# Kernel tuning notes

Measured on AMD Instinct MI355X. Metric: run time of the kernel, lower is better.

The kernel has to match this reference:

```python
import jax, jax.numpy as jnp
import numpy as np

HEADS = 16
DIM_HEAD = 64
SCALE = DIM_HEAD ** -0.5
MASK_NEG = 1000000.0


def setup_inputs() -> dict:
    key = jax.random.key(0)
    ks = jax.random.split(key, 6)
    B, N, M, D = 2, 2048, 2048, 1024
    inner = HEADS * DIM_HEAD  # 1024
    x = jax.random.normal(ks[0], (B, N, D), dtype=jnp.float32)
    context = jax.random.normal(ks[1], (B, M, D), dtype=jnp.float32)
    mask = jax.random.randint(ks[2], (B, N), 0, 2, dtype=jnp.int32)
    Wq = jax.random.normal(ks[3], (D, inner), dtype=jnp.float32) * (D ** -0.5)
    Wkv = jax.random.normal(ks[4], (D, 2 * inner), dtype=jnp.float32) * (D ** -0.5)
    Wout = jax.random.normal(ks[5], (inner, D), dtype=jnp.float32) * (inner ** -0.5)
    bout = jnp.zeros((D,), dtype=jnp.float32)
    return {"x": x, "context": context, "mask": mask,
            "Wq": Wq, "Wkv": Wkv, "Wout": Wout, "bout": bout}


def _split_heads(t):
    # [b, n, (h d)] -> [b, h, n, d]
    b, n, _ = t.shape
    return t.reshape(b, n, HEADS, DIM_HEAD).transpose(0, 2, 1, 3)


def reference(x, context, mask, Wq, Wkv, Wout, bout):
    kv = context @ Wkv                      # [b, m, 2*inner]
    k, v = jnp.split(kv, 2, axis=-1)
    q = x @ Wq                              # [b, n, inner]
    q, k, v = _split_heads(q), _split_heads(k), _split_heads(v)
    dots = jnp.einsum('bhnd,bhmd->bhnm', q, k) * SCALE
    # mask is [b, n]: additive penalty per query row (faithful to source)
    dots = dots - (1.0 - mask.astype(jnp.float32))[:, None, :, None] * MASK_NEG
    attn = jax.nn.softmax(dots, axis=-1)
    out = jnp.einsum('bhnm,bhmd->bhnd', attn, v)  # [b, h, n, d]
    b, h, n, d = out.shape
    out = out.transpose(0, 2, 1, 3).reshape(b, n, h * d)
    return out @ Wout + bout
```

## Files before the change

kernel.cpp:

```cpp
#include <hip/hip_runtime.h>
#include <hip/hip_bf16.h>
#include <math.h>

#define BATCH   2
#define NQ      2048
#define NKV     2048
#define DMODEL  1024
#define HEADS   16
#define INNER   1024
#define KVCOLS  2048

typedef short bf16x8 __attribute__((ext_vector_type(8)));
typedef float f32x4  __attribute__((ext_vector_type(4)));

__device__ __forceinline__ short f2bf(float x) {
    __hip_bfloat16 h = __float2bfloat16(x);
    return *reinterpret_cast<short*>(&h);
}
__device__ __forceinline__ float bf2f(short h) {
    unsigned int u = ((unsigned int)(unsigned short)h) << 16;
    float f;
    __builtin_memcpy(&f, &u, 4);
    return f;
}
__device__ __forceinline__ void gl_lds16(const void* g, void* l) {
    __builtin_amdgcn_global_load_lds(
        (const __attribute__((address_space(1))) unsigned int*)g,
        (__attribute__((address_space(3))) unsigned int*)l, 16, 0, 0);
}
__device__ __forceinline__ int sw(int row, int chunk) {
    return row * 64 + ((chunk ^ (row & 7)) << 3);
}

__global__ __launch_bounds__(256)
void split_cast(const float* __restrict__ in, short* __restrict__ hi,
                short* __restrict__ lo, int n)
{
    int i = (blockIdx.x * 256 + threadIdx.x) * 4;
    if (i >= n) return;
    float4 v = *(const float4*)(in + i);
    short4 h, l;
    h.x = f2bf(v.x); l.x = f2bf(v.x - bf2f(h.x));
    h.y = f2bf(v.y); l.y = f2bf(v.y - bf2f(h.y));
    h.z = f2bf(v.z); l.z = f2bf(v.z - bf2f(h.z));
    h.w = f2bf(v.w); l.w = f2bf(v.w - bf2f(h.w));
    *(short4*)(hi + i) = h;
    *(short4*)(lo + i) = l;
}

__device__ __forceinline__ void tile_transpose_split(
    const float* __restrict__ W, short* __restrict__ Wth, short* __restrict__ Wtl,
    int Kd, int Nd, int bx, int by, int split)
{
    __shared__ float t[32][33];
    const int lx = threadIdx.x & 31, ly = threadIdx.x >> 5;
    #pragma unroll
    for (int j = 0; j < 4; ++j)
        t[ly + j * 8][lx] = W[(size_t)(by * 32 + ly + j * 8) * Nd + bx * 32 + lx];
    __syncthreads();
    #pragma unroll
    for (int j = 0; j < 4; ++j) {
        const float v = t[lx][ly + j * 8];
        const short h = f2bf(v);
        const size_t idx = (size_t)(bx * 32 + ly + j * 8) * Kd + by * 32 + lx;
        Wth[idx] = h;
        if (split) Wtl[idx] = f2bf(v - bf2f(h));
    }
}

__global__ __launch_bounds__(256)
void prep_weights(const float* __restrict__ Wq, const float* __restrict__ Wkv,
                  const float* __restrict__ Wout,
                  short* __restrict__ WqTh, short* __restrict__ WqTl,
                  short* __restrict__ WkvTh, short* __restrict__ WkvTl,
                  short* __restrict__ WoutT)
{
    const int id = blockIdx.x;
    if (id < 1024) {
        tile_transpose_split(Wq, WqTh, WqTl, 1024, 1024, id & 31, id >> 5, 1);
    } else if (id < 3072) {
        const int r = id - 1024;
        tile_transpose_split(Wkv, WkvTh, WkvTl, 1024, 2048, r & 63, r >> 6, 1);
    } else {
        const int r = id - 3072;
        tile_transpose_split(Wout, WoutT, nullptr, 1024, 1024, r & 31, r >> 5, 0);
    }
}

template <int MODE>
__global__ __launch_bounds__(256)
void gemm3(const short* __restrict__ Ah, const short* __restrict__ Al,
           const short* __restrict__ Bth, const short* __restrict__ Btl,
           short* __restrict__ Chi, short* __restrict__ Clo,
           int Md, int Nd, int Kd)
{
    __shared__ short Ash[64 * 64];
    __shared__ short Asl[64 * 64];
    __shared__ short Bsh[64 * 64];
    __shared__ short Bsl[64 * 64];
    const int tid = threadIdx.x;
    const int m0 = blockIdx.y * 64, n0 = blockIdx.x * 64;
    const int w = tid >> 6, ln = tid & 63;
    const int wm = (w & 1) * 32, wn = (w >> 1) * 32;
    const int lr = ln & 15, lq = ln >> 4;

    f32x4 acc[2][2];
    #pragma unroll
    for (int mt = 0; mt < 2; ++mt)
        #pragma unroll
        for (int nt = 0; nt < 2; ++nt)
            #pragma unroll
            for (int r = 0; r < 4; ++r) acc[mt][nt][r] = 0.0f;

    for (int k0 = 0; k0 < Kd; k0 += 64) {
        __syncthreads();
        #pragma unroll
        for (int it = 0; it < 2; ++it) {
            const int f = it * 256 + tid;
            const int row = f >> 3, c8 = f & 7;
            gl_lds16(Ah  + (size_t)(m0 + row) * Kd + k0 + c8 * 8, Ash + f * 8);
            gl_lds16(Al  + (size_t)(m0 + row) * Kd + k0 + c8 * 8, Asl + f * 8);
            gl_lds16(Bth + (size_t)(n0 + row) * Kd + k0 + c8 * 8, Bsh + f * 8);
            gl_lds16(Btl + (size_t)(n0 + row) * Kd + k0 + c8 * 8, Bsl + f * 8);
        }
        __syncthreads();

        #pragma unroll
        for (int ks = 0; ks < 2; ++ks) {
            bf16x8 ah[2], al[2], bh[2], bl[2];
            #pragma unroll
            for (int t = 0; t < 2; ++t) {
                ah[t] = *(const bf16x8*)(Ash + (wm + t * 16 + lr) * 64 + ks * 32 + lq * 8);
                al[t] = *(const bf16x8*)(Asl + (wm + t * 16 + lr) * 64 + ks * 32 + lq * 8);
                bh[t] = *(const bf16x8*)(Bsh + (wn + t * 16 + lr) * 64 + ks * 32 + lq * 8);
                bl[t] = *(const bf16x8*)(Bsl + (wn + t * 16 + lr) * 64 + ks * 32 + lq * 8);
            }
            #pragma unroll
            for (int mt = 0; mt < 2; ++mt)
                #pragma unroll
                for (int nt = 0; nt < 2; ++nt) {
                    acc[mt][nt] = __builtin_amdgcn_mfma_f32_16x16x32_bf16(
                        ah[mt], bh[nt], acc[mt][nt], 0, 0, 0);
                    acc[mt][nt] = __builtin_amdgcn_mfma_f32_16x16x32_bf16(
                        ah[mt], bl[nt], acc[mt][nt], 0, 0, 0);
                    acc[mt][nt] = __builtin_amdgcn_mfma_f32_16x16x32_bf16(
                        al[mt], bh[nt], acc[mt][nt], 0, 0, 0);
                }
        }
    }

    #pragma unroll
    for (int mt = 0; mt < 2; ++mt)
        #pragma unroll
        for (int nt = 0; nt < 2; ++nt)
            #pragma unroll
            for (int r = 0; r < 4; ++r) {
                const int row = m0 + wm + mt * 16 + lq * 4 + r;
                const int col = n0 + wn + nt * 16 + lr;
                float v = acc[mt][nt][r];
                if (MODE == 1) v *= 0.125f;
                const short hh = f2bf(v);
                Chi[(size_t)row * Nd + col] = hh;
                Clo[(size_t)row * Nd + col] = f2bf(v - bf2f(hh));
            }
}

template <int FOUT>
__global__ __launch_bounds__(256)
void gemm1(const short* __restrict__ A, const short* __restrict__ Bt,
           void* __restrict__ Cv, int Md, int Nd, int Kd,
           const float* __restrict__ bias)
{
    __shared__ short As[64 * 64];
    __shared__ short Bs[64 * 64];
    const int tid = threadIdx.x;
    const int m0 = blockIdx.y * 64, n0 = blockIdx.x * 64;
    const int w = tid >> 6, ln = tid & 63;
    const int wm = (w & 1) * 32, wn = (w >> 1) * 32;
    const int lr = ln & 15, lq = ln >> 4;

    f32x4 acc[2][2];
    #pragma unroll
    for (int mt = 0; mt < 2; ++mt)
        #pragma unroll
        for (int nt = 0; nt < 2; ++nt)
            #pragma unroll
            for (int r = 0; r < 4; ++r) acc[mt][nt][r] = 0.0f;

    for (int k0 = 0; k0 < Kd; k0 += 64) {
        __syncthreads();
        #pragma unroll
        for (int it = 0; it < 2; ++it) {
            const int f = it * 256 + tid;
            const int row = f >> 3, c8 = f & 7;
            gl_lds16(A  + (size_t)(m0 + row) * Kd + k0 + c8 * 8, As + f * 8);
            gl_lds16(Bt + (size_t)(n0 + row) * Kd + k0 + c8 * 8, Bs + f * 8);
        }
        __syncthreads();
        #pragma unroll
        for (int ks = 0; ks < 2; ++ks) {
            bf16x8 af[2], bfr[2];
            #pragma unroll
            for (int t = 0; t < 2; ++t) {
                af[t]  = *(const bf16x8*)(As + (wm + t * 16 + lr) * 64 + ks * 32 + lq * 8);
                bfr[t] = *(const bf16x8*)(Bs + (wn + t * 16 + lr) * 64 + ks * 32 + lq * 8);
            }
            #pragma unroll
            for (int mt = 0; mt < 2; ++mt)
                #pragma unroll
                for (int nt = 0; nt < 2; ++nt)
                    acc[mt][nt] = __builtin_amdgcn_mfma_f32_16x16x32_bf16(
                        af[mt], bfr[nt], acc[mt][nt], 0, 0, 0);
        }
    }
    #pragma unroll
    for (int mt = 0; mt < 2; ++mt)
        #pragma unroll
        for (int nt = 0; nt < 2; ++nt)
            #pragma unroll
            for (int r = 0; r < 4; ++r) {
                const int row = m0 + wm + mt * 16 + lq * 4 + r;
                const int col = n0 + wn + nt * 16 + lr;
                if (FOUT == 1)
                    ((float*)Cv)[(size_t)row * Nd + col] = acc[mt][nt][r] + bias[col];
                else
                    ((short*)Cv)[(size_t)row * Nd + col] = f2bf(acc[mt][nt][r]);
            }
}

__global__ __launch_bounds__(512, 4)
void flash_v5(const short* __restrict__ qh, const short* __restrict__ ql,
              const short* __restrict__ kh, const short* __restrict__ kl,
              const short* __restrict__ vp, const int* __restrict__ mask,
              short* __restrict__ aob)
{
    const int qt = blockIdx.x, h = blockIdx.y, b = blockIdx.z;
    const int tid = threadIdx.x;
    const int w = tid >> 6, ln = tid & 63;
    const int lr = ln & 15, lq = ln >> 4;

    __shared__ short Kh[2 * 4096];
    __shared__ short Kl[2 * 4096];
    __shared__ short Vt[2 * 4096];
    __shared__ short Ps[128 * 64];

    const size_t qrow0 = (size_t)(b * NQ + qt * 128);

    bf16x8 aqh[2], aql[2];
    #pragma unroll
    for (int ks = 0; ks < 2; ++ks) {
        const size_t qoff = (qrow0 + w * 16 + lr) * INNER + h * 64 + ks * 32 + lq * 8;
        aqh[ks] = *(const bf16x8*)(qh + qoff);
        aql[ks] = *(const bf16x8*)(ql + qoff);
    }
    float keep[4];
    #pragma unroll
    for (int r = 0; r < 4; ++r)
        keep[r] = (float)mask[b * NQ + qt * 128 + w * 16 + lq * 4 + r];

    const int srow = tid >> 3, sc8 = tid & 7;
    const int kdst = sw(srow, sc8);
    const int kp = tid & 31, dg4 = (tid >> 5) * 4;
    int4 rkh, rkl; int2 rva, rvb;

    {
        const size_t koff = (size_t)(b * NKV + srow) * INNER + h * 64 + sc8 * 8;
        rkh = *(const int4*)(kh + koff);
        rkl = *(const int4*)(kl + koff);
        const short* v0 = vp + (size_t)(b * NKV + 2 * kp) * INNER + h * 64 + dg4;
        rva = *(const int2*)(v0);
        rvb = *(const int2*)(v0 + INNER);
        *(int4*)(Kh + kdst) = rkh;
        *(int4*)(Kl + kdst) = rkl;
        const short* as = (const short*)&rva;
        const short* bs = (const short*)&rvb;
        int* vt32 = (int*)Vt;
        #pragma unroll
        for (int j = 0; j < 4; ++j)
            vt32[(dg4 + j) * 32 + (((kp >> 2) ^ ((dg4 + j) & 7)) << 2) + (kp & 3)] =
                (int)((unsigned short)as[j] | ((unsigned int)(unsigned short)bs[j] << 16));
    }

    float psum[4];
    #pragma unroll
    for (int r = 0; r < 4; ++r) psum[r] = 0.0f;
    f32x4 oacc[4];
    #pragma unroll
    for (int dg = 0; dg < 4; ++dg)
        #pragma unroll
        for (int r = 0; r < 4; ++r) oacc[dg][r] = 0.0f;

    for (int kt = 0; kt < NKV / 64; ++kt) {
        const int cur = kt & 1;
        if (kt < NKV / 64 - 1) {
            const size_t krow0 = (size_t)(b * NKV + (kt + 1) * 64);
            const size_t koff = (krow0 + srow) * INNER + h * 64 + sc8 * 8;
            rkh = *(const int4*)(kh + koff);
            rkl = *(const int4*)(kl + koff);
            const short* v0 = vp + (krow0 + 2 * kp) * INNER + h * 64 + dg4;
            rva = *(const int2*)(v0);
            rvb = *(const int2*)(v0 + INNER);
        }
        __syncthreads();

        const short* KhC = Kh + cur * 4096;
        const short* KlC = Kl + cur * 4096;
        const short* VtC = Vt + cur * 4096;

        f32x4 sacc[4];
        #pragma unroll
        for (int g = 0; g < 4; ++g)
            #pragma unroll
            for (int r = 0; r < 4; ++r) sacc[g][r] = 0.0f;
        #pragma unroll
        for (int ks = 0; ks < 2; ++ks) {
            #pragma unroll
            for (int g = 0; g < 4; ++g) {
                const bf16x8 bkh = *(const bf16x8*)(KhC + sw(g * 16 + lr, ks * 4 + lq));
                const bf16x8 bkl = *(const bf16x8*)(KlC + sw(g * 16 + lr, ks * 4 + lq));
                sacc[g] = __builtin_amdgcn_mfma_f32_16x16x32_bf16(aqh[ks], bkh, sacc[g], 0, 0, 0);
                sacc[g] = __builtin_amdgcn_mfma_f32_16x16x32_bf16(aqh[ks], bkl, sacc[g], 0, 0, 0);
                sacc[g] = __builtin_amdgcn_mfma_f32_16x16x32_bf16(aql[ks], bkh, sacc[g], 0, 0, 0);
            }
        }

        #pragma unroll
        for (int r = 0; r < 4; ++r) {
            const int prow = w * 16 + lq * 4 + r;
            #pragma unroll
            for (int g = 0; g < 4; ++g) {
                float s = sacc[g][r];
                if (keep[r] == 0.0f) s = rintf(s * 16.0f) * 0.0625f;
                const float p = __expf(s);
                psum[r] += p;
                Ps[sw(prow, g * 2 + (lr >> 3)) + (lr & 7)] = f2bf(p);
            }
        }

        #pragma unroll
        for (int ks = 0; ks < 2; ++ks) {
            const bf16x8 ap = *(const bf16x8*)(Ps + sw(w * 16 + lr, ks * 4 + lq));
            #pragma unroll
            for (int dg = 0; dg < 4; ++dg) {
                const bf16x8 bv = *(const bf16x8*)(VtC + sw(dg * 16 + lr, ks * 4 + lq));
                oacc[dg] = __builtin_amdgcn_mfma_f32_16x16x32_bf16(ap, bv, oacc[dg], 0, 0, 0);
            }
        }

        if (kt < NKV / 64 - 1) {
            short* KhN = Kh + (cur ^ 1) * 4096;
            short* KlN = Kl + (cur ^ 1) * 4096;
            *(int4*)(KhN + kdst) = rkh;
            *(int4*)(KlN + kdst) = rkl;
            const short* as = (const short*)&rva;
            const short* bs = (const short*)&rvb;
            int* vt32 = (int*)(Vt + (cur ^ 1) * 4096);
            #pragma unroll
            for (int j = 0; j < 4; ++j)
                vt32[(dg4 + j) * 32 + (((kp >> 2) ^ ((dg4 + j) & 7)) << 2) + (kp & 3)] =
                    (int)((unsigned short)as[j] | ((unsigned int)(unsigned short)bs[j] << 16));
        }
    }

    #pragma unroll
    for (int off = 1; off < 16; off <<= 1)
        #pragma unroll
        for (int r = 0; r < 4; ++r)
            psum[r] += __shfl_xor(psum[r], off, 64);

    #pragma unroll
    for (int dg = 0; dg < 4; ++dg)
        #pragma unroll
        for (int r = 0; r < 4; ++r) {
            const int row = w * 16 + lq * 4 + r;
            aob[(qrow0 + row) * INNER + h * 64 + dg * 16 + lr] =
                f2bf(oacc[dg][r] / psum[r]);
        }
}

extern "C" void kernel_launch(void* const* d_in, const int* in_sizes, int n_in,
                              void* d_out, int out_size, void* d_ws, size_t ws_size,
                              hipStream_t stream)
{
    const float* x    = (const float*)d_in[0];
    const float* ctx  = (const float*)d_in[1];
    const int*   mask = (const int*)d_in[2];
    const float* Wq   = (const float*)d_in[3];
    const float* Wkv  = (const float*)d_in[4];
    const float* Wout = (const float*)d_in[5];
    const float* bout = (const float*)d_in[6];
    float* out = (float*)d_out;

    short* base  = (short*)d_ws;
    short* xh    = base;
    short* xl    = base + (size_t)4 * 1024 * 1024;
    short* ch    = xh;
    short* cl    = xl;
    short* vp    = xl;
    short* aob   = xh;
    short* WqTh  = base + (size_t) 8 * 1024 * 1024;
    short* WqTl  = base + (size_t) 9 * 1024 * 1024;
    short* qhp   = base + (size_t)10 * 1024 * 1024;
    short* qlp   = base + (size_t)14 * 1024 * 1024;
    short* WkvTh = base + (size_t)18 * 1024 * 1024;
    short* WkvTl = base + (size_t)20 * 1024 * 1024;
    short* khp   = base + (size_t)22 * 1024 * 1024;
    short* klp   = base + (size_t)26 * 1024 * 1024;
    short* WoutT = base + (size_t)30 * 1024 * 1024;

    const dim3 blk(256);
    split_cast<<<4096, blk, 0, stream>>>(x, xh, xl, 4096 * 1024);
    prep_weights<<<4096, blk, 0, stream>>>(Wq, Wkv, Wout,
                                           WqTh, WqTl, WkvTh, WkvTl, WoutT);
    gemm3<1><<<dim3(1024 / 64, 4096 / 64), blk, 0, stream>>>(
        xh, xl, WqTh, WqTl, qhp, qlp, 4096, 1024, 1024);
    split_cast<<<4096, blk, 0, stream>>>(ctx, ch, cl, 4096 * 1024);
    gemm3<0><<<dim3(1024 / 64, 4096 / 64), blk, 0, stream>>>(
        ch, cl, WkvTh, WkvTl, khp, klp, 4096, 1024, 1024);
    gemm1<0><<<dim3(1024 / 64, 4096 / 64), blk, 0, stream>>>(
        ch, WkvTh + (size_t)1024 * 1024, vp, 4096, 1024, 1024, nullptr);
    flash_v5<<<dim3(NQ / 128, HEADS, BATCH), dim3(512), 0, stream>>>(
        qhp, qlp, khp, klp, vp, mask, aob);
    gemm1<1><<<dim3(1024 / 64, 4096 / 64), blk, 0, stream>>>(
        aob, WoutT, out, 4096, 1024, 1024, bout);
}
```

Baseline: 308.7 us.

## Fuse prep kernels and batch Q/K/V projections into one larger-tile GEMM

Merges the two split_cast launches and the weight transpose into one prep kernel. Replaces three separate 64x64-tile projection GEMMs with a single launch that uses blockIdx.z to select Q, K or V. The new kernel uses 128x128 tiles with a 32-wide K step and an XOR-swizzled LDS layout, and V skips the low-part terms. Context and V get their own workspace buffers so the projections can run concurrently. This is meant to cut launch count, raise per-block data reuse and fill the GPU better, at the cost of more registers per thread (16 accumulators) and possibly lower occupancy.

```diff
diff --git a/kernel.cpp b/kernel.cpp
--- a/kernel.cpp
+++ b/kernel.cpp
@@ -32,12 +32,11 @@
     return row * 64 + ((chunk ^ (row & 7)) << 3);
 }
 
-__global__ __launch_bounds__(256)
-void split_cast(const float* __restrict__ in, short* __restrict__ hi,
-                short* __restrict__ lo, int n)
-{
-    int i = (blockIdx.x * 256 + threadIdx.x) * 4;
-    if (i >= n) return;
+__device__ __forceinline__ void split_chunk(const float* __restrict__ in,
+                                            short* __restrict__ hi,
+                                            short* __restrict__ lo, int id)
+{
+    const int i = (id * 256 + (int)threadIdx.x) * 4;
     float4 v = *(const float4*)(in + i);
     short4 h, l;
     h.x = f2bf(v.x); l.x = f2bf(v.x - bf2f(h.x));
@@ -69,78 +68,112 @@
 }
 
 __global__ __launch_bounds__(256)
-void prep_weights(const float* __restrict__ Wq, const float* __restrict__ Wkv,
-                  const float* __restrict__ Wout,
-                  short* __restrict__ WqTh, short* __restrict__ WqTl,
-                  short* __restrict__ WkvTh, short* __restrict__ WkvTl,
-                  short* __restrict__ WoutT)
+void prep_all(const float* __restrict__ x, const float* __restrict__ ctx,
+              const float* __restrict__ Wq, const float* __restrict__ Wkv,
+              const float* __restrict__ Wout,
+              short* __restrict__ xh, short* __restrict__ xl,
+              short* __restrict__ ch, short* __restrict__ cl,
+              short* __restrict__ WqTh, short* __restrict__ WqTl,
+              short* __restrict__ WkvTh, short* __restrict__ WkvTl,
+              short* __restrict__ WoutT)
 {
     const int id = blockIdx.x;
-    if (id < 1024) {
-        tile_transpose_split(Wq, WqTh, WqTl, 1024, 1024, id & 31, id >> 5, 1);
-    } else if (id < 3072) {
-        const int r = id - 1024;
-        tile_transpose_split(Wkv, WkvTh, WkvTl, 1024, 2048, r & 63, r >> 6, 1);
+    if (id < 4096) {
+        split_chunk(x, xh, xl, id);
+    } else if (id < 8192) {
+        split_chunk(ctx, ch, cl, id - 4096);
     } else {
-        const int r = id - 3072;
-        tile_transpose_split(Wout, WoutT, nullptr, 1024, 1024, r & 31, r >> 5, 0);
-    }
-}
-
-template <int MODE>
+        const int r = id - 8192;
+        if (r < 1024)
+            tile_transpose_split(Wq, WqTh, WqTl, 1024, 1024, r & 31, r >> 5, 1);
+        else if (r < 3072)
+            tile_transpose_split(Wkv, WkvTh, WkvTl, 1024, 2048, (r - 1024) & 63, (r - 1024) >> 6, 1);
+        else
+            tile_transpose_split(Wout, WoutT, nullptr, 1024, 1024, (r - 3072) & 31, (r - 3072) >> 5, 0);
+    }
+}
+
 __global__ __launch_bounds__(256)
-void gemm3(const short* __restrict__ Ah, const short* __restrict__ Al,
-           const short* __restrict__ Bth, const short* __restrict__ Btl,
-           short* __restrict__ Chi, short* __restrict__ Clo,
-           int Md, int Nd, int Kd)
-{
-    __shared__ short Ash[64 * 64];
-    __shared__ short Asl[64 * 64];
-    __shared__ short Bsh[64 * 64];
-    __shared__ short Bsl[64 * 64];
+void qkv_gemm(const short* __restrict__ xh, const short* __restrict__ xl,
+              const short* __restrict__ ch, const short* __restrict__ cl,
+              const short* __restrict__ WqTh, const short* __restrict__ WqTl,
+              const short* __restrict__ WkvTh, const short* __restrict__ WkvTl,
+              short* __restrict__ qhp, short* __restrict__ qlp,
+              short* __restrict__ khp, short* __restrict__ klp,
+              short* __restrict__ vp)
+{
+    __shared__ short Ash[128 * 32];
+    __shared__ short Asl[128 * 32];
+    __shared__ short Bsh[128 * 32];
+    __shared__ short Bsl[128 * 32];
+
     const int tid = threadIdx.x;
-    const int m0 = blockIdx.y * 64, n0 = blockIdx.x * 64;
+    const int z = blockIdx.z;
+    const int m0 = blockIdx.y * 128, n0 = blockIdx.x * 128;
     const int w = tid >> 6, ln = tid & 63;
-    const int wm = (w & 1) * 32, wn = (w >> 1) * 32;
+    const int wm = (w & 1) * 64, wn = (w >> 1) * 64;
     const int lr = ln & 15, lq = ln >> 4;
-
-    f32x4 acc[2][2];
-    #pragma unroll
-    for (int mt = 0; mt < 2; ++mt)
-        #pragma unroll
-        for (int nt = 0; nt < 2; ++nt)
+    const int terms = (z == 2) ? 1 : 3;
+
+    const short* Ah  = (z == 0) ? xh : ch;
+    const short* Al  = (z == 0) ? xl : cl;
+    const short* Bth = (z == 0) ? WqTh : (z == 1 ? WkvTh : WkvTh + (size_t)1024 * 1024);
+    const short* Btl = (z == 0) ? WqTl : WkvTl;
+
+    f32x4 acc[4][4];
+    #pragma unroll
+    for (int mt = 0; mt < 4; ++mt)
+        #pragma unroll
+        for (int nt = 0; nt < 4; ++nt)
             #pragma unroll
             for (int r = 0; r < 4; ++r) acc[mt][nt][r] = 0.0f;
 
-    for (int k0 = 0; k0 < Kd; k0 += 64) {
+    for (int k0 = 0; k0 < 1024; k0 += 32) {
         __syncthreads();
         #pragma unroll
         for (int it = 0; it < 2; ++it) {
             const int f = it * 256 + tid;
-            const int row = f >> 3, c8 = f & 7;
-            gl_lds16(Ah  + (size_t)(m0 + row) * Kd + k0 + c8 * 8, Ash + f * 8);
-            gl_lds16(Al  + (size_t)(m0 + row) * Kd + k0 + c8 * 8, Asl + f * 8);
-            gl_lds16(Bth + (size_t)(n0 + row) * Kd + k0 + c8 * 8, Bsh + f * 8);
-            gl_lds16(Btl + (size_t)(n0 + row) * Kd + k0 + c8 * 8, Bsl + f * 8);
+            const int row = f >> 2, c = f & 3;
+            const int cg = c ^ ((row >> 1) & 3);
+            const size_t ao = (size_t)(m0 + row) * 1024 + k0 + cg * 8;
+            const size_t bo = (size_t)(n0 + row) * 1024 + k0 + cg * 8;
+            gl_lds16(Ah  + ao, Ash + f * 8);
+            gl_lds16(Bth + bo, Bsh + f * 8);
+            if (terms == 3) {
+                gl_lds16(Al  + ao, Asl + f * 8);
+                gl_lds16(Btl + bo, Bsl + f * 8);
+            }
         }
         __syncthreads();
 
-        #pragma unroll
-        for (int ks = 0; ks < 2; ++ks) {
-            bf16x8 ah[2], al[2], bh[2], bl[2];
-            #pragma unroll
-            for (int t = 0; t < 2; ++t) {
-                ah[t] = *(const bf16x8*)(Ash + (wm + t * 16 + lr) * 64 + ks * 32 + lq * 8);
-                al[t] = *(const bf16x8*)(Asl + (wm + t * 16 + lr) * 64 + ks * 32 + lq * 8);
-                bh[t] = *(const bf16x8*)(Bsh + (wn + t * 16 + lr) * 64 + ks * 32 + lq * 8);
-                bl[t] = *(const bf16x8*)(Bsl + (wn + t * 16 + lr) * 64 + ks * 32 + lq * 8);
-            }
-            #pragma unroll
-            for (int mt = 0; mt < 2; ++mt)
+        bf16x8 ah[4], bh[4];
+        #pragma unroll
+        for (int t = 0; t < 4; ++t) {
+            const int ar = wm + t * 16 + lr;
+            const int br = wn + t * 16 + lr;
+            ah[t] = *(const bf16x8*)(Ash + ar * 32 + ((lq ^ ((ar >> 1) & 3)) << 3));
+            bh[t] = *(const bf16x8*)(Bsh + br * 32 + ((lq ^ ((br >> 1) & 3)) << 3));
+        }
+        #pragma unroll
+        for (int mt = 0; mt < 4; ++mt)
+            #pragma unroll
+            for (int nt = 0; nt < 4; ++nt)
+                acc[mt][nt] = __builtin_amdgcn_mfma_f32_16x16x32_bf16(
+                    ah[mt], bh[nt], acc[mt][nt], 0, 0, 0);
+
+        if (terms == 3) {
+            bf16x8 al[4], bl[4];
+            #pragma unroll
+            for (int t = 0; t < 4; ++t) {
+                const int ar = wm + t * 16 + lr;
+                const int br = wn + t * 16 + lr;
+                al[t] = *(const bf16x8*)(Asl + ar * 32 + ((lq ^ ((ar >> 1) & 3)) << 3));
+                bl[t] = *(const bf16x8*)(Bsl + br * 32 + ((lq ^ ((br >> 1) & 3)) << 3));
+            }
+            #pragma unroll
+            for (int mt = 0; mt < 4; ++mt)
                 #pragma unroll
-                for (int nt = 0; nt < 2; ++nt) {
-                    acc[mt][nt] = __builtin_amdgcn_mfma_f32_16x16x32_bf16(
-                        ah[mt], bh[nt], acc[mt][nt], 0, 0, 0);
+                for (int nt = 0; nt < 4; ++nt) {
                     acc[mt][nt] = __builtin_amdgcn_mfma_f32_16x16x32_bf16(
                         ah[mt], bl[nt], acc[mt][nt], 0, 0, 0);
                     acc[mt][nt] = __builtin_amdgcn_mfma_f32_16x16x32_bf16(
@@ -149,27 +182,29 @@
         }
     }
 
-    #pragma unroll
-    for (int mt = 0; mt < 2; ++mt)
-        #pragma unroll
-        for (int nt = 0; nt < 2; ++nt)
+    const float scale = (z == 0) ? 0.125f : 1.0f;
+    short* Chi = (z == 0) ? qhp : (z == 1 ? khp : vp);
+    short* Clo = (z == 0) ? qlp : klp;
+    #pragma unroll
+    for (int mt = 0; mt < 4; ++mt)
+        #pragma unroll
+        for (int nt = 0; nt < 4; ++nt)
             #pragma unroll
             for (int r = 0; r < 4; ++r) {
                 const int row = m0 + wm + mt * 16 + lq * 4 + r;
                 const int col = n0 + wn + nt * 16 + lr;
-                float v = acc[mt][nt][r];
-                if (MODE == 1) v *= 0.125f;
+                const float v = acc[mt][nt][r] * scale;
                 const short hh = f2bf(v);
-                Chi[(size_t)row * Nd + col] = hh;
-                Clo[(size_t)row * Nd + col] = f2bf(v - bf2f(hh));
-            }
-}
-
-template <int FOUT>
+                Chi[(size_t)row * 1024 + col] = hh;
+                if (z != 2)
+                    Clo[(size_t)row * 1024 + col] = f2bf(v - bf2f(hh));
+            }
+}
+
 __global__ __launch_bounds__(256)
-void gemm1(const short* __restrict__ A, const short* __restrict__ Bt,
-           void* __restrict__ Cv, int Md, int Nd, int Kd,
-           const float* __restrict__ bias)
+void gemm_out(const short* __restrict__ A, const short* __restrict__ Bt,
+              float* __restrict__ C, int Md, int Nd, int Kd,
+              const float* __restrict__ bias)
 {
     __shared__ short As[64 * 64];
     __shared__ short Bs[64 * 64];
@@ -221,10 +256,7 @@
             for (int r = 0; r < 4; ++r) {
                 const int row = m0 + wm + mt * 16 + lq * 4 + r;
                 const int col = n0 + wn + nt * 16 + lr;
-                if (FOUT == 1)
-                    ((float*)Cv)[(size_t)row * Nd + col] = acc[mt][nt][r] + bias[col];
-                else
-                    ((short*)Cv)[(size_t)row * Nd + col] = f2bf(acc[mt][nt][r]);
+                C[(size_t)row * Nd + col] = acc[mt][nt][r] + bias[col];
             }
 }
 
@@ -394,9 +426,6 @@
     short* base  = (short*)d_ws;
     short* xh    = base;
     short* xl    = base + (size_t)4 * 1024 * 1024;
-    short* ch    = xh;
-    short* cl    = xl;
-    short* vp    = xl;
     short* aob   = xh;
     short* WqTh  = base + (size_t) 8 * 1024 * 1024;
     short* WqTl  = base + (size_t) 9 * 1024 * 1024;
@@ -407,20 +436,19 @@
     short* khp   = base + (size_t)22 * 1024 * 1024;
     short* klp   = base + (size_t)26 * 1024 * 1024;
     short* WoutT = base + (size_t)30 * 1024 * 1024;
+    short* ch    = base + (size_t)31 * 1024 * 1024;
+    short* cl    = base + (size_t)35 * 1024 * 1024;
+    short* vp    = base + (size_t)39 * 1024 * 1024;
 
     const dim3 blk(256);
-    split_cast<<<4096, blk, 0, stream>>>(x, xh, xl, 4096 * 1024);
-    prep_weights<<<4096, blk, 0, stream>>>(Wq, Wkv, Wout,
-                                           WqTh, WqTl, WkvTh, WkvTl, WoutT);
-    gemm3<1><<<dim3(1024 / 64, 4096 / 64), blk, 0, stream>>>(
-        xh, xl, WqTh, WqTl, qhp, qlp, 4096, 1024, 1024);
-    split_cast<<<4096, blk, 0, stream>>>(ctx, ch, cl, 4096 * 1024);
-    gemm3<0><<<dim3(1024 / 64, 4096 / 64), blk, 0, stream>>>(
-        ch, cl, WkvTh, WkvTl, khp, klp, 4096, 1024, 1024);
-    gemm1<0><<<dim3(1024 / 64, 4096 / 64), blk, 0, stream>>>(
-        ch, WkvTh + (size_t)1024 * 1024, vp, 4096, 1024, 1024, nullptr);
+    prep_all<<<12288, blk, 0, stream>>>(x, ctx, Wq, Wkv, Wout,
+                                        xh, xl, ch, cl,
+                                        WqTh, WqTl, WkvTh, WkvTl, WoutT);
+    qkv_gemm<<<dim3(8, 32, 3), blk, 0, stream>>>(
+        xh, xl, ch, cl, WqTh, WqTl, WkvTh, WkvTl,
+        qhp, qlp, khp, klp, vp);
     flash_v5<<<dim3(NQ / 128, HEADS, BATCH), dim3(512), 0, stream>>>(
         qhp, qlp, khp, klp, vp, mask, aob);
-    gemm1<1><<<dim3(1024 / 64, 4096 / 64), blk, 0, stream>>>(
+    gemm_out<<<dim3(1024 / 64, 4096 / 64), blk, 0, stream>>>(
         aob, WoutT, out, 4096, 1024, 1024, bout);
 }
```

Measured after the change: 281.2 us. 8.9% less time.
